# Optimization experiments

Measured on AMD Instinct MI355X. Metric: run time of the kernel, lower is better.

Reference implementation:

```python
import jax, jax.numpy as jnp
import numpy as np

N = 100000      # nodes
E = 3200000     # edges
F_IN = 128      # num_features
H = 32          # hidden_dim (hard-coded in module)
C = 8           # num_classes
B = 128         # graphs in batch
BN_EPS = 1e-5


def setup_inputs() -> dict:
    key = jax.random.key(0)
    ks = jax.random.split(key, 24)
    s = 0.1
    inp = {
        "x": jax.random.normal(ks[0], (N, F_IN), jnp.float32),
        "edge_index": jax.random.randint(ks[1], (2, E), 0, N, dtype=jnp.int32),
        "batch": jnp.sort(jax.random.randint(ks[2], (N,), 0, B, dtype=jnp.int32)),
        # GINConv layer 0 (F_IN -> H -> H) MLP + BN params
        "w1_0": jax.random.normal(ks[3], (F_IN, H), jnp.float32) * s,
        "b1_0": jnp.zeros((H,), jnp.float32),
        "w2_0": jax.random.normal(ks[4], (H, H), jnp.float32) * s,
        "b2_0": jnp.zeros((H,), jnp.float32),
        "g_0": jnp.ones((H,), jnp.float32),
        "be_0": jnp.zeros((H,), jnp.float32),
        # GINConv layers 1..3 (H -> H -> H), stacked
        "w1s": jax.random.normal(ks[5], (3, H, H), jnp.float32) * s,
        "b1s": jnp.zeros((3, H), jnp.float32),
        "w2s": jax.random.normal(ks[6], (3, H, H), jnp.float32) * s,
        "b2s": jnp.zeros((3, H), jnp.float32),
        "gs": jnp.ones((3, H), jnp.float32),
        "bes": jnp.zeros((3, H), jnp.float32),
        # classifier head
        "fc1_w": jax.random.normal(ks[7], (H, H), jnp.float32) * s,
        "fc1_b": jnp.zeros((H,), jnp.float32),
        "fc2_w": jax.random.normal(ks[8], (H, C), jnp.float32) * s,
        "fc2_b": jnp.zeros((C,), jnp.float32),
    }
    return inp


def _gin_conv(h, src, dst, w1, b1, w2, b2):
    # GINConv with eps=0: MLP((1+eps)*x + sum_{j in N(i)} x_j)
    agg = jax.ops.segment_sum(h[src], dst, num_segments=N)  # scatter-add aggregation
    z = h + agg
    return jnp.maximum(z @ w1 + b1, 0.0) @ w2 + b2


def _batch_norm(h, gamma, beta):
    # BatchNorm1d in training mode: batch stats over node dim, biased variance
    mean = h.mean(axis=0)
    var = jnp.mean(jnp.square(h - mean), axis=0)
    return gamma * (h - mean) * jax.lax.rsqrt(var + BN_EPS) + beta


def reference(x, edge_index, batch, w1_0, b1_0, w2_0, b2_0, g_0, be_0,
              w1s, b1s, w2s, b2s, gs, bes, fc1_w, fc1_b, fc2_w, fc2_b):
    src, dst = edge_index[0], edge_index[1]
    h = _batch_norm(jnp.maximum(_gin_conv(x, src, dst, w1_0, b1_0, w2_0, b2_0), 0.0), g_0, be_0)
    for i in range(3):  # fixed small layer loop
        h = _batch_norm(jnp.maximum(_gin_conv(h, src, dst, w1s[i], b1s[i], w2s[i], b2s[i]), 0.0), gs[i], bes[i])
    # global_mean_pool over batch ids
    counts = jax.ops.segment_sum(jnp.ones((N,), h.dtype), batch, num_segments=B)
    pooled = jax.ops.segment_sum(h, batch, num_segments=B) / jnp.maximum(counts, 1.0)[:, None]
    h = jnp.maximum(pooled @ fc1_w + fc1_b, 0.0)
    # dropout p=0.5 treated as identity (eval-mode determinism)
    logits = h @ fc2_w + fc2_b
    return jax.nn.log_softmax(logits, axis=-1)
```

## Files before the change

kernel.cpp:

```cpp
#include <hip/hip_runtime.h>
#include <hip/hip_bf16.h>

#define NN   100000
#define EE   3200000
#define HH   32
#define BB   128
#define KMAX 96
#define LSTRIDE 97
#define NBKT 256
#define BSPAN 391
#define WSPAN 98
#define EBLK 256
#define CHUNK 12500

static constexpr size_t Q_OFF      = 0;
static constexpr size_t AGG_OFF    = 6400000;
static constexpr size_t H_OFF      = 19200000;
static constexpr size_t EPACK_OFF  = 32000000;
static constexpr size_t SRC_OFF    = 44800000;
static constexpr size_t OFF_OFF    = 57600000;
static constexpr size_t HIST_OFF   = 58100000;
static constexpr size_t START_OFF  = 58400000;
static constexpr size_t BBASE_OFF  = 58700000;
static constexpr size_t STATS_OFF  = 58710000;
static constexpr size_t POOLED_OFF = 58711024;
static constexpr size_t PCNT_OFF   = 58727408;
static constexpr size_t ZERO_OFF   = STATS_OFF;
static constexpr size_t ZERO_BYTES = 17920;

__global__ __launch_bounds__(256) void hist_kernel(const int* __restrict__ ei,
                                                   int* __restrict__ hist) {
    __shared__ int lh[NBKT];
    int tid = threadIdx.x, blk = blockIdx.x;
    for (int i = tid; i < NBKT; i += 256) lh[i] = 0;
    __syncthreads();
    int e0 = blk * CHUNK;
    for (int e = e0 + tid; e < e0 + CHUNK; e += 256) {
        int d = ei[EE + e];
        atomicAdd(&lh[d / BSPAN], 1);
    }
    __syncthreads();
    for (int i = tid; i < NBKT; i += 256) hist[blk * NBKT + i] = lh[i];
}

__global__ __launch_bounds__(NBKT) void bucket_scan_kernel(const int* __restrict__ hist,
                                                           int* __restrict__ bbase,
                                                           int* __restrict__ start) {
    __shared__ int sm[NBKT];
    int t = threadIdx.x;
    int mine = 0;
    for (int blk = 0; blk < EBLK; blk++) mine += hist[blk * NBKT + t];
    sm[t] = mine;
    __syncthreads();
    for (int off = 1; off < NBKT; off <<= 1) {
        int v = (t >= off) ? sm[t - off] : 0;
        __syncthreads();
        sm[t] += v;
        __syncthreads();
    }
    int base = sm[t] - mine;
    bbase[t] = base;
    if (t == NBKT - 1) bbase[NBKT] = sm[t];
    int run = base;
    for (int blk = 0; blk < EBLK; blk++) {
        start[blk * NBKT + t] = run;
        run += hist[blk * NBKT + t];
    }
}

__global__ __launch_bounds__(256) void scatter_kernel(const int* __restrict__ ei,
                                                      const int* __restrict__ start,
                                                      int* __restrict__ epack) {
    __shared__ int loff[NBKT];
    int tid = threadIdx.x, blk = blockIdx.x;
    for (int i = tid; i < NBKT; i += 256) loff[i] = start[blk * NBKT + i];
    __syncthreads();
    int e0 = blk * CHUNK;
    for (int e = e0 + tid; e < e0 + CHUNK; e += 256) {
        int s = ei[e];
        int d = ei[EE + e];
        int b = d / BSPAN;
        int slot = atomicAdd(&loff[b], 1);
        epack[slot] = s | ((d - b * BSPAN) << 17);
    }
}

__global__ __launch_bounds__(256) void csr_compact_kernel(const int* __restrict__ epack,
                                                          const int* __restrict__ bbase,
                                                          int* __restrict__ off,
                                                          int* __restrict__ srcs) {
    __shared__ int lcnt[WSPAN];
    __shared__ int lbase[WSPAN + 1];
    __shared__ int lcsr[WSPAN * LSTRIDE];
    __shared__ int sh_before;
    int blk = blockIdx.x;
    int b = blk >> 2, w = blk & 3;
    int base = b * BSPAN;
    int span = NN - base;
    if (span <= 0) return;
    if (span > BSPAN) span = BSPAN;
    int wstart = w * WSPAN;
    if (wstart >= span) return;
    int wend = min(wstart + WSPAN, span);
    int wn = wend - wstart;
    int tid = threadIdx.x;
    if (tid == 0) sh_before = 0;
    for (int i = tid; i < wn; i += 256) lcnt[i] = 0;
    __syncthreads();
    int p0 = bbase[b], p1 = bbase[b + 1];
    int nbefore = 0;
    for (int i = p0 + tid; i < p1; i += 256) {
        int wd = epack[i];
        int ld = wd >> 17;
        if (ld < wstart) nbefore++;
        else if (ld < wend) {
            int slot = atomicAdd(&lcnt[ld - wstart], 1);
            if (slot < KMAX) lcsr[(ld - wstart) * LSTRIDE + slot] = wd & 0x1FFFF;
        }
    }
    atomicAdd(&sh_before, nbefore);
    __syncthreads();
    if (tid == 0) {
        int run = 0;
        for (int i = 0; i < wn; i++) { lbase[i] = run; run += min(lcnt[i], KMAX); }
        lbase[wn] = run;
    }
    __syncthreads();
    int w0 = p0 + sh_before;
    for (int i = tid; i < wn; i += 256) off[base + wstart + i] = w0 + lbase[i];
    if (base + wend == NN && tid == 0) off[NN] = w0 + lbase[wn];
    int m = lbase[wn];
    for (int j = tid; j < m; j += 256) {
        int lo = 0, hi = wn - 1;
        while (lo < hi) {
            int mid = (lo + hi + 1) >> 1;
            if (lbase[mid] <= j) lo = mid; else hi = mid - 1;
        }
        srcs[w0 + j] = lcsr[lo * LSTRIDE + (j - lbase[lo])];
    }
}

__device__ __forceinline__ unsigned bf16rn(float f) {
    unsigned b = __float_as_uint(f);
    return (b + 0x7fffu + ((b >> 16) & 1u)) >> 16;
}

__device__ __forceinline__ void acc_row(float* a, uint4 v) {
    a[0] += __uint_as_float(v.x << 16);
    a[1] += __uint_as_float(v.x & 0xffff0000u);
    a[2] += __uint_as_float(v.y << 16);
    a[3] += __uint_as_float(v.y & 0xffff0000u);
    a[4] += __uint_as_float(v.z << 16);
    a[5] += __uint_as_float(v.z & 0xffff0000u);
    a[6] += __uint_as_float(v.w << 16);
    a[7] += __uint_as_float(v.w & 0xffff0000u);
}

template <int FIN>
__global__ __launch_bounds__(256) void proj_kernel(const float* __restrict__ hin,
                                                   const float* __restrict__ w1,
                                                   const float* __restrict__ stats_prev,
                                                   const float* __restrict__ gamma,
                                                   const float* __restrict__ beta,
                                                   uint4* __restrict__ q4) {
    constexpr int JC = FIN / 4;
    __shared__ float sa[32], sc[32];
    __shared__ float part[4 * 64 * 33];
    int tid = threadIdx.x;
    if constexpr (FIN == 32) {
        if (tid < 32) {
            float mean = stats_prev[tid] * (1.0f / NN);
            float var  = fmaxf(stats_prev[32 + tid] * (1.0f / NN) - mean * mean, 0.f);
            float av = gamma[tid] * rsqrtf(var + 1e-5f);
            sa[tid] = av;
            sc[tid] = beta[tid] - mean * av;
        }
        __syncthreads();
    }
    int wv = __builtin_amdgcn_readfirstlane(tid >> 6);
    int ln = tid & 63;
    int n = blockIdx.x * 64 + ln;
    float acc[32];
#pragma unroll
    for (int c = 0; c < 32; c++) acc[c] = 0.f;
    if (n < NN) {
        const float4* h4 = (const float4*)(hin + (size_t)n * FIN + wv * JC);
        float hv[JC];
#pragma unroll
        for (int k = 0; k < JC / 4; k++) {
            float4 v = h4[k];
            hv[4*k] = v.x; hv[4*k+1] = v.y; hv[4*k+2] = v.z; hv[4*k+3] = v.w;
        }
        if constexpr (FIN == 32) {
#pragma unroll
            for (int j = 0; j < JC; j++) hv[j] = fmaf(hv[j], sa[wv * JC + j], sc[wv * JC + j]);
        }
#pragma unroll 4
        for (int j = 0; j < JC; j++) {
            float hvj = hv[j];
            const float* wrow = w1 + (size_t)(wv * JC + j) * 32;
#pragma unroll
            for (int c = 0; c < 32; c++) acc[c] = fmaf(hvj, wrow[c], acc[c]);
        }
    }
    float* my = part + (wv * 64 + ln) * 33;
#pragma unroll
    for (int c = 0; c < 32; c++) my[c] = acc[c];
    __syncthreads();
    int node = tid >> 2, p = tid & 3;
    int n2 = blockIdx.x * 64 + node;
    if (n2 >= NN) return;
    float r[8];
#pragma unroll
    for (int k = 0; k < 8; k++) {
        int c = p * 8 + k;
        r[k] = (part[(0 * 64 + node) * 33 + c] + part[(1 * 64 + node) * 33 + c])
             + (part[(2 * 64 + node) * 33 + c] + part[(3 * 64 + node) * 33 + c]);
    }
    uint4 u;
    u.x = bf16rn(r[0]) | (bf16rn(r[1]) << 16);
    u.y = bf16rn(r[2]) | (bf16rn(r[3]) << 16);
    u.z = bf16rn(r[4]) | (bf16rn(r[5]) << 16);
    u.w = bf16rn(r[6]) | (bf16rn(r[7]) << 16);
    q4[(size_t)n2 * 4 + p] = u;
}

__global__ __launch_bounds__(256) void gather_kernel(const uint4* __restrict__ q4,
                                                     const int* __restrict__ srcs,
                                                     const int* __restrict__ off,
                                                     const float* __restrict__ b1,
                                                     float* __restrict__ agg) {
    int t = blockIdx.x * 256 + threadIdx.x;
    int n = t >> 2;
    if (n >= NN) return;
    int p = t & 3;
    float a[8];
#pragma unroll
    for (int k = 0; k < 8; k++) a[k] = b1[p * 8 + k];
    acc_row(a, q4[(size_t)n * 4 + p]);
    int o0 = off[n];
    int d = off[n + 1] - o0;
    const int* lst = srcs + o0;
    int i = 0;
    for (; i + 8 <= d; i += 8) {
        int s0 = __builtin_nontemporal_load(lst + i);
        int s1 = __builtin_nontemporal_load(lst + i + 1);
        int s2 = __builtin_nontemporal_load(lst + i + 2);
        int s3 = __builtin_nontemporal_load(lst + i + 3);
        int s4 = __builtin_nontemporal_load(lst + i + 4);
        int s5 = __builtin_nontemporal_load(lst + i + 5);
        int s6 = __builtin_nontemporal_load(lst + i + 6);
        int s7 = __builtin_nontemporal_load(lst + i + 7);
        uint4 v0 = q4[(size_t)s0 * 4 + p];
        uint4 v1 = q4[(size_t)s1 * 4 + p];
        uint4 v2 = q4[(size_t)s2 * 4 + p];
        uint4 v3 = q4[(size_t)s3 * 4 + p];
        uint4 v4 = q4[(size_t)s4 * 4 + p];
        uint4 v5 = q4[(size_t)s5 * 4 + p];
        uint4 v6 = q4[(size_t)s6 * 4 + p];
        uint4 v7 = q4[(size_t)s7 * 4 + p];
        acc_row(a, v0); acc_row(a, v1); acc_row(a, v2); acc_row(a, v3);
        acc_row(a, v4); acc_row(a, v5); acc_row(a, v6); acc_row(a, v7);
    }
    for (; i < d; i++) {
        int s = __builtin_nontemporal_load(lst + i);
        acc_row(a, q4[(size_t)s * 4 + p]);
    }
    float4* ar = (float4*)(agg + (size_t)n * 32 + p * 8);
    float4 f0, f1;
    f0.x = a[0]; f0.y = a[1]; f0.z = a[2]; f0.w = a[3];
    f1.x = a[4]; f1.y = a[5]; f1.z = a[6]; f1.w = a[7];
    ar[0] = f0; ar[1] = f1;
}

__global__ __launch_bounds__(256) void mlp_kernel(const float* __restrict__ agg,
                                                  const float* __restrict__ w2,
                                                  const float* __restrict__ b2,
                                                  float* __restrict__ r,
                                                  float* __restrict__ stats) {
    __shared__ float tile[256 * 33];
    __shared__ float ps[8 * 32];
    __shared__ float pq[8 * 32];
    int tid = threadIdx.x;
    int n = blockIdx.x * 256 + tid;
    float rc[32];
    if (n < NN) {
        float u[32];
        const float4* a4 = (const float4*)(agg + (size_t)n * 32);
#pragma unroll
        for (int k = 0; k < 8; k++) {
            float4 v = a4[k];
            u[4*k]   = fmaxf(v.x, 0.f);
            u[4*k+1] = fmaxf(v.y, 0.f);
            u[4*k+2] = fmaxf(v.z, 0.f);
            u[4*k+3] = fmaxf(v.w, 0.f);
        }
#pragma unroll
        for (int c = 0; c < 32; c++) rc[c] = b2[c];
#pragma unroll 4
        for (int j = 0; j < 32; j++) {
            float uj = u[j];
            const float* wrow = w2 + (size_t)j * 32;
#pragma unroll
            for (int c = 0; c < 32; c++) rc[c] = fmaf(uj, wrow[c], rc[c]);
        }
#pragma unroll
        for (int c = 0; c < 32; c++) rc[c] = fmaxf(rc[c], 0.f);
        float4* rr = (float4*)(r + (size_t)n * 32);
#pragma unroll
        for (int k = 0; k < 8; k++) {
            float4 v; v.x = rc[4*k]; v.y = rc[4*k+1]; v.z = rc[4*k+2]; v.w = rc[4*k+3];
            rr[k] = v;
        }
    } else {
#pragma unroll
        for (int c = 0; c < 32; c++) rc[c] = 0.f;
    }
#pragma unroll
    for (int c = 0; c < 32; c++) tile[tid * 33 + c] = rc[c];
    __syncthreads();
    {
        int c = tid & 31, rb = tid >> 5;
        float s = 0.f, sq = 0.f;
        for (int it = 0; it < 32; it++) {
            float v = tile[(rb * 32 + it) * 33 + c];
            s += v; sq += v * v;
        }
        ps[rb * 32 + c] = s; pq[rb * 32 + c] = sq;
    }
    __syncthreads();
    if (tid < 32) {
        float s = 0.f, sq = 0.f;
#pragma unroll
        for (int rb = 0; rb < 8; rb++) { s += ps[rb * 32 + tid]; sq += pq[rb * 32 + tid]; }
        atomicAdd(&stats[tid], s);
        atomicAdd(&stats[32 + tid], sq);
    }
}

#define PR 16
__global__ __launch_bounds__(256) void pool_kernel(const float* __restrict__ h,
                                                   const int* __restrict__ batch,
                                                   float* __restrict__ pooled,
                                                   float* __restrict__ pcnt) {
    int t = blockIdx.x * 256 + threadIdx.x;
    int c = t & 31;
    int g = t >> 5;
    int r0 = g * PR;
    if (r0 >= NN) return;
    int r1 = min(r0 + PR, NN);
    int cur = batch[r0];
    float acc = 0.f, cn = 0.f;
    for (int rr = r0; rr < r1; rr++) {
        int b = batch[rr];
        if (b != cur) {
            atomicAdd(&pooled[cur * 32 + c], acc);
            if (c == 0) atomicAdd(&pcnt[cur], cn);
            acc = 0.f; cn = 0.f; cur = b;
        }
        acc += h[(size_t)rr * 32 + c];
        cn += 1.f;
    }
    atomicAdd(&pooled[cur * 32 + c], acc);
    if (c == 0) atomicAdd(&pcnt[cur], cn);
}

__global__ __launch_bounds__(128) void head_kernel(const float* __restrict__ pooled,
                                                   const float* __restrict__ pcnt,
                                                   const float* __restrict__ stats3,
                                                   const float* __restrict__ g3,
                                                   const float* __restrict__ be3,
                                                   const float* __restrict__ fc1w,
                                                   const float* __restrict__ fc1b,
                                                   const float* __restrict__ fc2w,
                                                   const float* __restrict__ fc2b,
                                                   float* __restrict__ out) {
    __shared__ float sa[32], sc[32];
    int g = threadIdx.x;
    if (g < 32) {
        float mean = stats3[g] * (1.0f / NN);
        float var  = fmaxf(stats3[32 + g] * (1.0f / NN) - mean * mean, 0.f);
        float av = g3[g] * rsqrtf(var + 1e-5f);
        sa[g] = av;
        sc[g] = be3[g] - mean * av;
    }
    __syncthreads();
    if (g >= BB) return;
    float inv = 1.f / fmaxf(pcnt[g], 1.f);
    float xv[32];
#pragma unroll
    for (int c = 0; c < 32; c++) xv[c] = fmaf(sa[c], pooled[g * 32 + c] * inv, sc[c]);
    float u[32];
#pragma unroll 4
    for (int k = 0; k < 32; k++) {
        float s = fc1b[k];
#pragma unroll
        for (int c = 0; c < 32; c++) s = fmaf(xv[c], fc1w[c * 32 + k], s);
        u[k] = fmaxf(s, 0.f);
    }
    float l[8];
#pragma unroll
    for (int o = 0; o < 8; o++) {
        float s = fc2b[o];
#pragma unroll
        for (int k = 0; k < 32; k++) s = fmaf(u[k], fc2w[k * 8 + o], s);
        l[o] = s;
    }
    float m = l[0];
#pragma unroll
    for (int o = 1; o < 8; o++) m = fmaxf(m, l[o]);
    float se = 0.f;
#pragma unroll
    for (int o = 0; o < 8; o++) se += expf(l[o] - m);
    float lse = logf(se) + m;
#pragma unroll
    for (int o = 0; o < 8; o++) out[g * 8 + o] = l[o] - lse;
}

extern "C" void kernel_launch(void* const* d_in, const int* in_sizes, int n_in,
                              void* d_out, int out_size, void* d_ws, size_t ws_size,
                              hipStream_t stream) {
    const float* x    = (const float*)d_in[0];
    const int*   ei   = (const int*)d_in[1];
    const int*   batch= (const int*)d_in[2];
    const float* w1_0 = (const float*)d_in[3];
    const float* b1_0 = (const float*)d_in[4];
    const float* w2_0 = (const float*)d_in[5];
    const float* b2_0 = (const float*)d_in[6];
    const float* g_0  = (const float*)d_in[7];
    const float* be_0 = (const float*)d_in[8];
    const float* w1s  = (const float*)d_in[9];
    const float* b1s  = (const float*)d_in[10];
    const float* w2s  = (const float*)d_in[11];
    const float* b2s  = (const float*)d_in[12];
    const float* gs   = (const float*)d_in[13];
    const float* bes  = (const float*)d_in[14];
    const float* fc1w = (const float*)d_in[15];
    const float* fc1b = (const float*)d_in[16];
    const float* fc2w = (const float*)d_in[17];
    const float* fc2b = (const float*)d_in[18];
    float* out = (float*)d_out;

    char* ws = (char*)d_ws;
    uint4*    q4     = (uint4*)(ws + Q_OFF);
    float*    agg    = (float*)(ws + AGG_OFF);
    float*    h      = (float*)(ws + H_OFF);
    int*      epack  = (int*)(ws + EPACK_OFF);
    int*      srcs   = (int*)(ws + SRC_OFF);
    int*      off    = (int*)(ws + OFF_OFF);
    int*      hist   = (int*)(ws + HIST_OFF);
    int*      start  = (int*)(ws + START_OFF);
    int*      bbase  = (int*)(ws + BBASE_OFF);
    float*    stats  = (float*)(ws + STATS_OFF);
    float*    pooled = (float*)(ws + POOLED_OFF);
    float*    pcnt   = (float*)(ws + PCNT_OFF);

    (void)hipMemsetAsync(ws + ZERO_OFF, 0, ZERO_BYTES, stream);

    hist_kernel<<<EBLK, 256, 0, stream>>>(ei, hist);
    bucket_scan_kernel<<<1, NBKT, 0, stream>>>(hist, bbase, start);
    scatter_kernel<<<EBLK, 256, 0, stream>>>(ei, start, epack);
    csr_compact_kernel<<<NBKT * 4, 256, 0, stream>>>(epack, bbase, off, srcs);

    const int pblk = (NN + 63) / 64;
    const int nblk = (NN + 255) / 256;
    const int gblk = (NN * 4 + 255) / 256;

    proj_kernel<128><<<pblk, 256, 0, stream>>>(x, w1_0, nullptr, nullptr, nullptr, q4);
    gather_kernel<<<gblk, 256, 0, stream>>>(q4, srcs, off, b1_0, agg);
    mlp_kernel<<<nblk, 256, 0, stream>>>(agg, w2_0, b2_0, h, stats);

    for (int i = 0; i < 3; i++) {
        const float* st_prev = stats + i * 64;
        proj_kernel<32><<<pblk, 256, 0, stream>>>(h, w1s + i * 1024, st_prev,
                                                  gs + i * 32, bes + i * 32, q4);
        gather_kernel<<<gblk, 256, 0, stream>>>(q4, srcs, off, b1s + i * 32, agg);
        mlp_kernel<<<nblk, 256, 0, stream>>>(agg, w2s + i * 1024, b2s + i * 32, h,
                                             stats + (i + 1) * 64);
    }

    int pthreads = ((NN + PR - 1) / PR) * 32;
    pool_kernel<<<(pthreads + 255) / 256, 256, 0, stream>>>(h, batch, pooled, pcnt);
    head_kernel<<<1, 128, 0, stream>>>(pooled, pcnt, stats + 3 * 64, gs + 2 * 32,
                                       bes + 2 * 32, fc1w, fc1b, fc2w, fc2b, out);
}
```

Before: 592.1 us.

## Fuse neighbor gather with second MLP layer and BN stats accumulation

Merges the gather and MLP kernels into one kernel. Each group of four threads assembles the full 32-wide post-ReLU row through lane shuffles, then computes its 8 output columns against a transposed W2 held in shared memory. This removes the write and re-read of the 12.8 MB fp32 agg buffer and one launch per layer. In exchange, BN statistics now go through per-element shared-memory atomics, which may contend, and every block reloads W2 into shared memory.

Result: slower. 721.6 us (+21.9%).

```diff
diff --git a/kernel.cpp b/kernel.cpp
--- a/kernel.cpp
+++ b/kernel.cpp
@@ -14,17 +14,16 @@
 #define CHUNK 12500
 
 static constexpr size_t Q_OFF      = 0;
-static constexpr size_t AGG_OFF    = 6400000;
-static constexpr size_t H_OFF      = 19200000;
-static constexpr size_t EPACK_OFF  = 32000000;
-static constexpr size_t SRC_OFF    = 44800000;
-static constexpr size_t OFF_OFF    = 57600000;
-static constexpr size_t HIST_OFF   = 58100000;
-static constexpr size_t START_OFF  = 58400000;
-static constexpr size_t BBASE_OFF  = 58700000;
-static constexpr size_t STATS_OFF  = 58710000;
-static constexpr size_t POOLED_OFF = 58711024;
-static constexpr size_t PCNT_OFF   = 58727408;
+static constexpr size_t H_OFF      = 6400000;
+static constexpr size_t EPACK_OFF  = 19200000;
+static constexpr size_t SRC_OFF    = 32000000;
+static constexpr size_t OFF_OFF    = 44800000;
+static constexpr size_t HIST_OFF   = 45300000;
+static constexpr size_t START_OFF  = 45600000;
+static constexpr size_t BBASE_OFF  = 45900000;
+static constexpr size_t STATS_OFF  = 45910000;
+static constexpr size_t POOLED_OFF = 45911024;
+static constexpr size_t PCNT_OFF   = 45927408;
 static constexpr size_t ZERO_OFF   = STATS_OFF;
 static constexpr size_t ZERO_BYTES = 17920;
 
@@ -225,117 +224,106 @@
     q4[(size_t)n2 * 4 + p] = u;
 }
 
-__global__ __launch_bounds__(256) void gather_kernel(const uint4* __restrict__ q4,
-                                                     const int* __restrict__ srcs,
-                                                     const int* __restrict__ off,
-                                                     const float* __restrict__ b1,
-                                                     float* __restrict__ agg) {
-    int t = blockIdx.x * 256 + threadIdx.x;
+__global__ __launch_bounds__(256) void gmlp_kernel(const uint4* __restrict__ q4,
+                                                   const int* __restrict__ srcs,
+                                                   const int* __restrict__ off,
+                                                   const float* __restrict__ b1,
+                                                   const float* __restrict__ w2,
+                                                   const float* __restrict__ b2,
+                                                   float* __restrict__ hout,
+                                                   float* __restrict__ stats) {
+    __shared__ float w2t[32 * 33];
+    __shared__ float sacc[64];
+    int tid = threadIdx.x;
+    for (int i = tid; i < 1024; i += 256) w2t[(i & 31) * 33 + (i >> 5)] = w2[i];
+    if (tid < 64) sacc[tid] = 0.f;
+    __syncthreads();
+
+    int t = blockIdx.x * 256 + tid;
     int n = t >> 2;
-    if (n >= NN) return;
     int p = t & 3;
-    float a[8];
-#pragma unroll
-    for (int k = 0; k < 8; k++) a[k] = b1[p * 8 + k];
-    acc_row(a, q4[(size_t)n * 4 + p]);
-    int o0 = off[n];
-    int d = off[n + 1] - o0;
-    const int* lst = srcs + o0;
-    int i = 0;
-    for (; i + 8 <= d; i += 8) {
-        int s0 = __builtin_nontemporal_load(lst + i);
-        int s1 = __builtin_nontemporal_load(lst + i + 1);
-        int s2 = __builtin_nontemporal_load(lst + i + 2);
-        int s3 = __builtin_nontemporal_load(lst + i + 3);
-        int s4 = __builtin_nontemporal_load(lst + i + 4);
-        int s5 = __builtin_nontemporal_load(lst + i + 5);
-        int s6 = __builtin_nontemporal_load(lst + i + 6);
-        int s7 = __builtin_nontemporal_load(lst + i + 7);
-        uint4 v0 = q4[(size_t)s0 * 4 + p];
-        uint4 v1 = q4[(size_t)s1 * 4 + p];
-        uint4 v2 = q4[(size_t)s2 * 4 + p];
-        uint4 v3 = q4[(size_t)s3 * 4 + p];
-        uint4 v4 = q4[(size_t)s4 * 4 + p];
-        uint4 v5 = q4[(size_t)s5 * 4 + p];
-        uint4 v6 = q4[(size_t)s6 * 4 + p];
-        uint4 v7 = q4[(size_t)s7 * 4 + p];
-        acc_row(a, v0); acc_row(a, v1); acc_row(a, v2); acc_row(a, v3);
-        acc_row(a, v4); acc_row(a, v5); acc_row(a, v6); acc_row(a, v7);
-    }
-    for (; i < d; i++) {
-        int s = __builtin_nontemporal_load(lst + i);
-        acc_row(a, q4[(size_t)s * 4 + p]);
-    }
-    float4* ar = (float4*)(agg + (size_t)n * 32 + p * 8);
-    float4 f0, f1;
-    f0.x = a[0]; f0.y = a[1]; f0.z = a[2]; f0.w = a[3];
-    f1.x = a[4]; f1.y = a[5]; f1.z = a[6]; f1.w = a[7];
-    ar[0] = f0; ar[1] = f1;
-}
-
-__global__ __launch_bounds__(256) void mlp_kernel(const float* __restrict__ agg,
-                                                  const float* __restrict__ w2,
-                                                  const float* __restrict__ b2,
-                                                  float* __restrict__ r,
-                                                  float* __restrict__ stats) {
-    __shared__ float tile[256 * 33];
-    __shared__ float ps[8 * 32];
-    __shared__ float pq[8 * 32];
-    int tid = threadIdx.x;
-    int n = blockIdx.x * 256 + tid;
-    float rc[32];
     if (n < NN) {
-        float u[32];
-        const float4* a4 = (const float4*)(agg + (size_t)n * 32);
-#pragma unroll
-        for (int k = 0; k < 8; k++) {
-            float4 v = a4[k];
-            u[4*k]   = fmaxf(v.x, 0.f);
-            u[4*k+1] = fmaxf(v.y, 0.f);
-            u[4*k+2] = fmaxf(v.z, 0.f);
-            u[4*k+3] = fmaxf(v.w, 0.f);
-        }
-#pragma unroll
-        for (int c = 0; c < 32; c++) rc[c] = b2[c];
+        float a[8];
+#pragma unroll
+        for (int k = 0; k < 8; k++) a[k] = b1[p * 8 + k];
+        acc_row(a, q4[(size_t)n * 4 + p]);
+        int o0 = off[n];
+        int d = off[n + 1] - o0;
+        const int* lst = srcs + o0;
+        int i = 0;
+        for (; i + 8 <= d; i += 8) {
+            int s0 = __builtin_nontemporal_load(lst + i);
+            int s1 = __builtin_nontemporal_load(lst + i + 1);
+            int s2 = __builtin_nontemporal_load(lst + i + 2);
+            int s3 = __builtin_nontemporal_load(lst + i + 3);
+            int s4 = __builtin_nontemporal_load(lst + i + 4);
+            int s5 = __builtin_nontemporal_load(lst + i + 5);
+            int s6 = __builtin_nontemporal_load(lst + i + 6);
+            int s7 = __builtin_nontemporal_load(lst + i + 7);
+            uint4 v0 = q4[(size_t)s0 * 4 + p];
+            uint4 v1 = q4[(size_t)s1 * 4 + p];
+            uint4 v2 = q4[(size_t)s2 * 4 + p];
+            uint4 v3 = q4[(size_t)s3 * 4 + p];
+            uint4 v4 = q4[(size_t)s4 * 4 + p];
+            uint4 v5 = q4[(size_t)s5 * 4 + p];
+            uint4 v6 = q4[(size_t)s6 * 4 + p];
+            uint4 v7 = q4[(size_t)s7 * 4 + p];
+            acc_row(a, v0); acc_row(a, v1); acc_row(a, v2); acc_row(a, v3);
+            acc_row(a, v4); acc_row(a, v5); acc_row(a, v6); acc_row(a, v7);
+        }
+        for (; i < d; i++) {
+            int s = __builtin_nontemporal_load(lst + i);
+            acc_row(a, q4[(size_t)s * 4 + p]);
+        }
+        float um[8];
+#pragma unroll
+        for (int k = 0; k < 8; k++) um[k] = fmaxf(a[k], 0.f);
+        float u16[16];
+        {
+            int half = p & 1;
+#pragma unroll
+            for (int k = 0; k < 8; k++) {
+                float o = __shfl_xor(um[k], 1);
+                u16[half * 8 + k] = um[k];
+                u16[(half ^ 1) * 8 + k] = o;
+            }
+        }
+        float u32v[32];
+        {
+            int halfq = (p >> 1) & 1;
+#pragma unroll
+            for (int k = 0; k < 16; k++) {
+                float o = __shfl_xor(u16[k], 2);
+                u32v[halfq * 16 + k] = u16[k];
+                u32v[(halfq ^ 1) * 16 + k] = o;
+            }
+        }
+        float v[8];
+#pragma unroll
+        for (int k = 0; k < 8; k++) v[k] = b2[p * 8 + k];
 #pragma unroll 4
         for (int j = 0; j < 32; j++) {
-            float uj = u[j];
-            const float* wrow = w2 + (size_t)j * 32;
-#pragma unroll
-            for (int c = 0; c < 32; c++) rc[c] = fmaf(uj, wrow[c], rc[c]);
-        }
-#pragma unroll
-        for (int c = 0; c < 32; c++) rc[c] = fmaxf(rc[c], 0.f);
-        float4* rr = (float4*)(r + (size_t)n * 32);
+            float uj = u32v[j];
+#pragma unroll
+            for (int k = 0; k < 8; k++)
+                v[k] = fmaf(uj, w2t[(p * 8 + k) * 33 + j], v[k]);
+        }
+        float r[8];
+#pragma unroll
+        for (int k = 0; k < 8; k++) r[k] = fmaxf(v[k], 0.f);
+        float4* hr = (float4*)(hout + (size_t)n * 32 + p * 8);
+        float4 f0, f1;
+        f0.x = r[0]; f0.y = r[1]; f0.z = r[2]; f0.w = r[3];
+        f1.x = r[4]; f1.y = r[5]; f1.z = r[6]; f1.w = r[7];
+        hr[0] = f0; hr[1] = f1;
 #pragma unroll
         for (int k = 0; k < 8; k++) {
-            float4 v; v.x = rc[4*k]; v.y = rc[4*k+1]; v.z = rc[4*k+2]; v.w = rc[4*k+3];
-            rr[k] = v;
-        }
-    } else {
-#pragma unroll
-        for (int c = 0; c < 32; c++) rc[c] = 0.f;
-    }
-#pragma unroll
-    for (int c = 0; c < 32; c++) tile[tid * 33 + c] = rc[c];
-    __syncthreads();
-    {
-        int c = tid & 31, rb = tid >> 5;
-        float s = 0.f, sq = 0.f;
-        for (int it = 0; it < 32; it++) {
-            float v = tile[(rb * 32 + it) * 33 + c];
-            s += v; sq += v * v;
-        }
-        ps[rb * 32 + c] = s; pq[rb * 32 + c] = sq;
-    }
-    __syncthreads();
-    if (tid < 32) {
-        float s = 0.f, sq = 0.f;
-#pragma unroll
-        for (int rb = 0; rb < 8; rb++) { s += ps[rb * 32 + tid]; sq += pq[rb * 32 + tid]; }
-        atomicAdd(&stats[tid], s);
-        atomicAdd(&stats[32 + tid], sq);
-    }
+            atomicAdd(&sacc[p * 8 + k], r[k]);
+            atomicAdd(&sacc[32 + p * 8 + k], r[k] * r[k]);
+        }
+    }
+    __syncthreads();
+    if (tid < 64) atomicAdd(&stats[tid], sacc[tid]);
 }
 
 #define PR 16
@@ -443,7 +431,6 @@
 
     char* ws = (char*)d_ws;
     uint4*    q4     = (uint4*)(ws + Q_OFF);
-    float*    agg    = (float*)(ws + AGG_OFF);
     float*    h      = (float*)(ws + H_OFF);
     int*      epack  = (int*)(ws + EPACK_OFF);
     int*      srcs   = (int*)(ws + SRC_OFF);
@@ -463,20 +450,18 @@
     csr_compact_kernel<<<NBKT * 4, 256, 0, stream>>>(epack, bbase, off, srcs);
 
     const int pblk = (NN + 63) / 64;
-    const int nblk = (NN + 255) / 256;
     const int gblk = (NN * 4 + 255) / 256;
 
     proj_kernel<128><<<pblk, 256, 0, stream>>>(x, w1_0, nullptr, nullptr, nullptr, q4);
-    gather_kernel<<<gblk, 256, 0, stream>>>(q4, srcs, off, b1_0, agg);
-    mlp_kernel<<<nblk, 256, 0, stream>>>(agg, w2_0, b2_0, h, stats);
+    gmlp_kernel<<<gblk, 256, 0, stream>>>(q4, srcs, off, b1_0, w2_0, b2_0, h, stats);
 
     for (int i = 0; i < 3; i++) {
         const float* st_prev = stats + i * 64;
         proj_kernel<32><<<pblk, 256, 0, stream>>>(h, w1s + i * 1024, st_prev,
                                                   gs + i * 32, bes + i * 32, q4);
-        gather_kernel<<<gblk, 256, 0, stream>>>(q4, srcs, off, b1s + i * 32, agg);
-        mlp_kernel<<<nblk, 256, 0, stream>>>(agg, w2s + i * 1024, b2s + i * 32, h,
-                                             stats + (i + 1) * 64);
+        gmlp_kernel<<<gblk, 256, 0, stream>>>(q4, srcs, off, b1s + i * 32,
+                                              w2s + i * 1024, b2s + i * 32, h,
+                                              stats + (i + 1) * 64);
     }
 
     int pthreads = ((NN + PR - 1) / PR) * 32;
```

## Add per-bucket rescatter by window and source quarter before CSR compaction

Applied to the files above, without the earlier changes.

Adds a rescatter kernel that sorts each destination bucket's packed edges by a key built from the destination sub-window and the source-index quarter. It writes them to a second buffer along with per-key offsets. The CSR compaction blocks now read only their own window's edges instead of scanning the whole bucket, and no longer need the 'before' count. Within each destination's neighbor list, sources end up roughly grouped by index range, which may help gather locality. The cost is an extra read-and-write pass over all edges and more workspace.

Result: no change. 595.0 us (+0.5%).

```diff
diff --git a/kernel.cpp b/kernel.cpp
--- a/kernel.cpp
+++ b/kernel.cpp
@@ -10,6 +10,7 @@
 #define NBKT 256
 #define BSPAN 391
 #define WSPAN 98
+#define QS   25000
 #define EBLK 256
 #define CHUNK 12500
 
@@ -17,14 +18,16 @@
 static constexpr size_t AGG_OFF    = 6400000;
 static constexpr size_t H_OFF      = 19200000;
 static constexpr size_t EPACK_OFF  = 32000000;
-static constexpr size_t SRC_OFF    = 44800000;
-static constexpr size_t OFF_OFF    = 57600000;
-static constexpr size_t HIST_OFF   = 58100000;
-static constexpr size_t START_OFF  = 58400000;
-static constexpr size_t BBASE_OFF  = 58700000;
-static constexpr size_t STATS_OFF  = 58710000;
-static constexpr size_t POOLED_OFF = 58711024;
-static constexpr size_t PCNT_OFF   = 58727408;
+static constexpr size_t EPACK2_OFF = 44800000;
+static constexpr size_t SRC_OFF    = 57600000;
+static constexpr size_t OFF_OFF    = 70400000;
+static constexpr size_t HIST_OFF   = 70900000;
+static constexpr size_t START_OFF  = 71200000;
+static constexpr size_t BBASE_OFF  = 71500000;
+static constexpr size_t KB2_OFF    = 71510000;
+static constexpr size_t STATS_OFF  = 71530000;
+static constexpr size_t POOLED_OFF = 71531024;
+static constexpr size_t PCNT_OFF   = 71547408;
 static constexpr size_t ZERO_OFF   = STATS_OFF;
 static constexpr size_t ZERO_BYTES = 17920;
 
@@ -85,14 +88,47 @@
     }
 }
 
-__global__ __launch_bounds__(256) void csr_compact_kernel(const int* __restrict__ epack,
-                                                          const int* __restrict__ bbase,
+__global__ __launch_bounds__(256) void rescatter_kernel(const int* __restrict__ epack,
+                                                        const int* __restrict__ bbase,
+                                                        int* __restrict__ epack2,
+                                                        int* __restrict__ kb2) {
+    __shared__ int lh[16];
+    __shared__ int lofs[17];
+    __shared__ int lrun[16];
+    int b = blockIdx.x, tid = threadIdx.x;
+    if (tid < 16) lh[tid] = 0;
+    __syncthreads();
+    int p0 = bbase[b], p1 = bbase[b + 1];
+    for (int i = p0 + tid; i < p1; i += 256) {
+        int wd = epack[i];
+        int key = ((wd >> 17) / WSPAN) * 4 + (wd & 0x1FFFF) / QS;
+        atomicAdd(&lh[key], 1);
+    }
+    __syncthreads();
+    if (tid == 0) {
+        int run = p0;
+        for (int k = 0; k < 16; k++) { lofs[k] = run; run += lh[k]; }
+        lofs[16] = run;
+    }
+    __syncthreads();
+    if (tid < 17) kb2[b * 17 + tid] = lofs[tid];
+    if (tid < 16) lrun[tid] = lofs[tid];
+    __syncthreads();
+    for (int i = p0 + tid; i < p1; i += 256) {
+        int wd = epack[i];
+        int key = ((wd >> 17) / WSPAN) * 4 + (wd & 0x1FFFF) / QS;
+        int slot = atomicAdd(&lrun[key], 1);
+        epack2[slot] = wd;
+    }
+}
+
+__global__ __launch_bounds__(256) void csr_compact_kernel(const int* __restrict__ epack2,
+                                                          const int* __restrict__ kb2,
                                                           int* __restrict__ off,
                                                           int* __restrict__ srcs) {
     __shared__ int lcnt[WSPAN];
     __shared__ int lbase[WSPAN + 1];
     __shared__ int lcsr[WSPAN * LSTRIDE];
-    __shared__ int sh_before;
     int blk = blockIdx.x;
     int b = blk >> 2, w = blk & 3;
     int base = b * BSPAN;
@@ -104,21 +140,15 @@
     int wend = min(wstart + WSPAN, span);
     int wn = wend - wstart;
     int tid = threadIdx.x;
-    if (tid == 0) sh_before = 0;
     for (int i = tid; i < wn; i += 256) lcnt[i] = 0;
     __syncthreads();
-    int p0 = bbase[b], p1 = bbase[b + 1];
-    int nbefore = 0;
-    for (int i = p0 + tid; i < p1; i += 256) {
-        int wd = epack[i];
-        int ld = wd >> 17;
-        if (ld < wstart) nbefore++;
-        else if (ld < wend) {
-            int slot = atomicAdd(&lcnt[ld - wstart], 1);
-            if (slot < KMAX) lcsr[(ld - wstart) * LSTRIDE + slot] = wd & 0x1FFFF;
-        }
-    }
-    atomicAdd(&sh_before, nbefore);
+    int p0w = kb2[b * 17 + w * 4], p1w = kb2[b * 17 + w * 4 + 4];
+    for (int i = p0w + tid; i < p1w; i += 256) {
+        int wd = epack2[i];
+        int ld = (wd >> 17) - wstart;
+        int slot = atomicAdd(&lcnt[ld], 1);
+        if (slot < KMAX) lcsr[ld * LSTRIDE + slot] = wd & 0x1FFFF;
+    }
     __syncthreads();
     if (tid == 0) {
         int run = 0;
@@ -126,9 +156,8 @@
         lbase[wn] = run;
     }
     __syncthreads();
-    int w0 = p0 + sh_before;
-    for (int i = tid; i < wn; i += 256) off[base + wstart + i] = w0 + lbase[i];
-    if (base + wend == NN && tid == 0) off[NN] = w0 + lbase[wn];
+    for (int i = tid; i < wn; i += 256) off[base + wstart + i] = p0w + lbase[i];
+    if (base + wend == NN && tid == 0) off[NN] = p0w + lbase[wn];
     int m = lbase[wn];
     for (int j = tid; j < m; j += 256) {
         int lo = 0, hi = wn - 1;
@@ -136,7 +165,7 @@
             int mid = (lo + hi + 1) >> 1;
             if (lbase[mid] <= j) lo = mid; else hi = mid - 1;
         }
-        srcs[w0 + j] = lcsr[lo * LSTRIDE + (j - lbase[lo])];
+        srcs[p0w + j] = lcsr[lo * LSTRIDE + (j - lbase[lo])];
     }
 }
 
@@ -446,11 +475,13 @@
     float*    agg    = (float*)(ws + AGG_OFF);
     float*    h      = (float*)(ws + H_OFF);
     int*      epack  = (int*)(ws + EPACK_OFF);
+    int*      epack2 = (int*)(ws + EPACK2_OFF);
     int*      srcs   = (int*)(ws + SRC_OFF);
     int*      off    = (int*)(ws + OFF_OFF);
     int*      hist   = (int*)(ws + HIST_OFF);
     int*      start  = (int*)(ws + START_OFF);
     int*      bbase  = (int*)(ws + BBASE_OFF);
+    int*      kb2    = (int*)(ws + KB2_OFF);
     float*    stats  = (float*)(ws + STATS_OFF);
     float*    pooled = (float*)(ws + POOLED_OFF);
     float*    pcnt   = (float*)(ws + PCNT_OFF);
@@ -460,7 +491,8 @@
     hist_kernel<<<EBLK, 256, 0, stream>>>(ei, hist);
     bucket_scan_kernel<<<1, NBKT, 0, stream>>>(hist, bbase, start);
     scatter_kernel<<<EBLK, 256, 0, stream>>>(ei, start, epack);
-    csr_compact_kernel<<<NBKT * 4, 256, 0, stream>>>(epack, bbase, off, srcs);
+    rescatter_kernel<<<NBKT, 256, 0, stream>>>(epack, bbase, epack2, kb2);
+    csr_compact_kernel<<<NBKT * 4, 256, 0, stream>>>(epack2, kb2, off, srcs);
 
     const int pblk = (NN + 63) / 64;
     const int nblk = (NN + 255) / 256;
```
